# Kernel tuning notes

Hardware: AMD Instinct MI355X
Metric: run time of the kernel (lower is better)

The kernel has to match this reference:

```python
import jax, jax.numpy as jnp
import numpy as np
import math

S, B, H, NH = 2048, 2, 2048, 16
HN = H // NH  # 128, head dim


def _rope_cache(seq_len, hn):
    # inv_freqs over even indices, half_hn entries
    inv_freqs = 0.0001 ** (jnp.arange(0, hn, 2, dtype=jnp.float32) / hn)
    pos = jnp.arange(seq_len, dtype=jnp.float32)
    angles = pos[:, None] * inv_freqs  # [s, hn/2]
    return jnp.cos(angles), jnp.sin(angles)


def _apply_rope(x, cos, sin):
    # x: [s, b, np, hn]; cos/sin: [s, hn/2] broadcast over b, np
    half = x.shape[-1] // 2
    c = cos[:, None, None, :]
    s = sin[:, None, None, :]
    left, right = x[..., :half], x[..., half:]
    return jnp.concatenate((c * left - s * right, s * left + c * right), axis=-1)


def setup_inputs() -> dict:
    key = jax.random.key(0)
    k0, k1, k2 = jax.random.split(key, 3)
    hidden_states = jax.random.normal(k0, (S, B, H), dtype=jnp.float32)
    # causal additive mask, broadcast over batch and heads
    causal = jnp.tril(jnp.ones((S, S), dtype=bool))
    attention_mask = jnp.where(causal, 0.0, -1e9).astype(jnp.float32)[None, None]
    W_qkv = jax.random.normal(k1, (3 * H, H), dtype=jnp.float32) * 0.02
    b_qkv = jnp.zeros((3 * H,), dtype=jnp.float32)
    W_dense = jax.random.normal(k2, (H, H), dtype=jnp.float32) * 0.02
    b_dense = jnp.zeros((H,), dtype=jnp.float32)
    return {"hidden_states": hidden_states, "attention_mask": attention_mask,
            "W_qkv": W_qkv, "b_qkv": b_qkv, "W_dense": W_dense, "b_dense": b_dense}


def reference(hidden_states, attention_mask, W_qkv, b_qkv, W_dense, b_dense):
    s, b, h = hidden_states.shape
    # fused QKV projection: [s,b,3h] -> [s,b,np,3*hn] -> split per head
    mixed = hidden_states @ W_qkv.T + b_qkv
    mixed = mixed.reshape(s, b, NH, 3 * HN)
    q, k, v = jnp.split(mixed, 3, axis=-1)  # each [s,b,np,hn]
    cos, sin = _rope_cache(s, HN)
    q = _apply_rope(q, cos, sin)
    k = _apply_rope(k, cos, sin)
    norm_factor = math.sqrt(HN)  # coeff is None (scale_attn_by_inverse_layer_idx=False)
    scores = jnp.einsum('sbnh,tbnh->bnst', q, k) / norm_factor  # [b,np,sq,sk]
    scores = scores + attention_mask
    probs = jax.nn.softmax(scores, axis=-1)  # dropout p=0 in eval
    ctx = jnp.einsum('bnst,tbnh->sbnh', probs, v).reshape(s, b, h)
    return ctx @ W_dense.T + b_dense  # [s,b,h]
```

## Files before the change

kernel.cpp:

```cpp
#include <hip/hip_runtime.h>

#define SEQ   2048
#define BATCH 2
#define HID   2048
#define NHEAD 16
#define HDIM  128
#define MTOT  4096
#define KDIM  2048

typedef __attribute__((ext_vector_type(8))) short  bf16x8;
typedef __attribute__((ext_vector_type(4))) float  f32x4;
typedef __attribute__((ext_vector_type(4))) unsigned short u16x4;
typedef __attribute__((ext_vector_type(8))) unsigned short u16x8;

__device__ __forceinline__ unsigned short f2bf(float x) {
  unsigned u = __float_as_uint(x);
  u += 0x7fffu + ((u >> 16) & 1u);
  return (unsigned short)(u >> 16);
}

__device__ __forceinline__ float fexp2(float x) {
  float r;
  asm("v_exp_f32 %0, %1" : "=v"(r) : "v"(x));
  return r;
}

__device__ __forceinline__ void gl_lds16(const void* g, void* l) {
  __builtin_amdgcn_global_load_lds(
      (__attribute__((address_space(1))) void*)g,
      (__attribute__((address_space(3))) void*)l, 16, 0, 0);
}

__device__ __forceinline__ f32x4 mfma16(bf16x8 a, bf16x8 b, f32x4 c) {
  return __builtin_amdgcn_mfma_f32_16x16x32_bf16(a, b, c, 0, 0, 0);
}

__global__ __launch_bounds__(256, 8)
void prep(const float* __restrict__ hidden, const float* __restrict__ Wqkv,
          const float* __restrict__ Wd,
          unsigned short* __restrict__ hidb, unsigned short* __restrict__ wqkvb,
          unsigned short* __restrict__ wdb,
          float* __restrict__ cosT, float* __restrict__ sinT) {
  int bid = blockIdx.x;
  if (bid < 24576) {
    const float* src; unsigned short* dst; int lb;
    if (bid < 8192)       { src = hidden; dst = hidb;  lb = bid; }
    else if (bid < 20480) { src = Wqkv;   dst = wqkvb; lb = bid - 8192; }
    else                  { src = Wd;     dst = wdb;   lb = bid - 20480; }
    int i = lb * 256 + threadIdx.x;
    int base = i << 2;
    int r = base >> 11, k = base & 2047;
    f32x4 v = *(const f32x4*)(src + base);
    int kp = k ^ (((r >> 1) & 3) << 3);
    u16x4 o;
    o[0] = f2bf(v[0]); o[1] = f2bf(v[1]); o[2] = f2bf(v[2]); o[3] = f2bf(v[3]);
    *(u16x4*)(dst + (size_t)r * 2048 + kp) = o;
  } else {
    int idx = (bid - 24576) * 256 + threadIdx.x;
    int s = idx >> 6, i = idx & 63;
    float inv = powf(1e-4f, (float)i * (1.0f / 64.0f));
    float a = (float)s * inv;
    cosT[idx] = cosf(a);
    sinT[idx] = sinf(a);
  }
}

__global__ __launch_bounds__(512, 2)
void gemm_qkv(const unsigned short* __restrict__ A,
              const unsigned short* __restrict__ Bt,
              const float* __restrict__ bias,
              unsigned short* __restrict__ Qs,
              unsigned short* __restrict__ Ks,
              unsigned short* __restrict__ Vp,
              const float* __restrict__ cosT,
              const float* __restrict__ sinT)
{
  __shared__ alignas(16) char lds[98304];
  const int tid = threadIdx.x;
  const int wid = tid >> 6, lane = tid & 63, g = lane >> 4, c = lane & 15;
  const int wr = wid >> 2, wc = wid & 3;

  const int bid = blockIdx.x;
  const int swz = (bid & 7) * 64 + (bid >> 3);
  const int nblk = swz & 15, mblk = swz >> 4;
  const int m0 = mblk << 7;
  const int n0 = nblk * 384;
  const int nh = nblk;

  char* ldsb = (char*)lds;
  const int slotg = (g ^ ((c >> 1) & 3)) << 4;
  const char* ldsAr = ldsb + (wr * 64 + c) * 64 + slotg;
  const char* ldsBr = ldsb + 24576 + (wc * 16 + c) * 64 + slotg;

  const char* gA = (const char*)A  + (size_t)(m0 + (tid >> 2)) * 4096 + (tid & 3) * 16;
  const char* gB = (const char*)Bt + (size_t)(n0 + (tid >> 2)) * 4096 + (tid & 3) * 16;
  char* lA = ldsb + tid * 16;
  char* lB = ldsb + 24576 + tid * 16;

#define STG_A(T, BUF) gl_lds16(gA + (T) * 64, lA + (BUF) * 8192)
#define STG_B(T, BUF) do { const char* _g = gB + (T) * 64; char* _l = lB + (BUF) * 24576; \
    gl_lds16(_g, _l); gl_lds16(_g + 524288, _l + 8192); gl_lds16(_g + 1048576, _l + 16384); } while (0)

  f32x4 acc[4][6];
#pragma unroll
  for (int i = 0; i < 4; ++i)
#pragma unroll
    for (int j = 0; j < 6; ++j) {
      acc[i][j][0] = 0.f; acc[i][j][1] = 0.f; acc[i][j][2] = 0.f; acc[i][j][3] = 0.f;
    }

  bf16x8 a[4], b[6];
  const int NT = KDIM / 32;

#define TILE(T, BUF, BUFN) do {                                             \
    if ((T) + 2 < NT) { STG_A((T) + 2, BUFN); STG_B((T) + 2, BUFN); }       \
    _Pragma("unroll")                                                       \
    for (int mf = 0; mf < 4; ++mf)                                          \
      a[mf] = *(const bf16x8*)(ldsAr + (BUF) * 8192 + mf * 1024);           \
    _Pragma("unroll")                                                       \
    for (int nl = 0; nl < 6; ++nl)                                          \
      b[nl] = *(const bf16x8*)(ldsBr + (BUF) * 24576 + nl * 4096);          \
    __builtin_amdgcn_s_setprio(1);                                          \
    _Pragma("unroll")                                                       \
    for (int mf = 0; mf < 4; ++mf)                                          \
      _Pragma("unroll")                                                     \
      for (int nl = 0; nl < 6; ++nl)                                        \
        acc[mf][nl] = mfma16(a[mf], b[nl], acc[mf][nl]);                    \
    __builtin_amdgcn_s_setprio(0);                                          \
    if ((T) + 2 < NT) { asm volatile("s_waitcnt vmcnt(4)" ::: "memory"); }  \
    else              { asm volatile("s_waitcnt vmcnt(0)" ::: "memory"); }  \
    __builtin_amdgcn_s_barrier();                                           \
  } while (0)

  STG_A(0, 0); STG_B(0, 0);
  STG_A(1, 1); STG_B(1, 1);
  asm volatile("s_waitcnt vmcnt(4)" ::: "memory");
  __builtin_amdgcn_s_barrier();

  for (int t = 0; t < 63; t += 3) {
    TILE(t, 0, 2);
    TILE(t + 1, 1, 0);
    TILE(t + 2, 2, 1);
  }
  TILE(63, 0, 2);

  const float qsc = 0.08838834764831845f * 1.4426950408889634f;
  const int dl = wc * 16 + c;
#pragma unroll
  for (int ar = 0; ar < 4; ++ar) {
#pragma unroll
    for (int rr = 0; rr < 4; ++rr) {
      int m = m0 + wr * 64 + ar * 16 + g * 4 + rr;
      int s = m >> 1, bb = m & 1;
      size_t plane = (size_t)(bb * NHEAD + nh) * (SEQ * HDIM);
      int swb = (s & 7) << 3;
      float co = cosT[s * 64 + dl], si = sinT[s * 64 + dl];
      {
        float xl = acc[ar][0][rr] + bias[n0 + dl];
        float xr = acc[ar][1][rr] + bias[n0 + 64 + dl];
        Qs[plane + (size_t)s * HDIM + (dl ^ swb)]        = f2bf((co * xl - si * xr) * qsc);
        Qs[plane + (size_t)s * HDIM + ((dl + 64) ^ swb)] = f2bf((si * xl + co * xr) * qsc);
      }
      {
        float xl = acc[ar][2][rr] + bias[n0 + 128 + dl];
        float xr = acc[ar][3][rr] + bias[n0 + 192 + dl];
        Ks[plane + (size_t)s * HDIM + (dl ^ swb)]        = f2bf(co * xl - si * xr);
        Ks[plane + (size_t)s * HDIM + ((dl + 64) ^ swb)] = f2bf(si * xl + co * xr);
      }
      Vp[plane + (size_t)s * HDIM + dl]      = f2bf(acc[ar][4][rr] + bias[n0 + 256 + dl]);
      Vp[plane + (size_t)s * HDIM + dl + 64] = f2bf(acc[ar][5][rr] + bias[n0 + 320 + dl]);
    }
  }
#undef TILE
#undef STG_A
#undef STG_B
}

__global__ __launch_bounds__(512, 2)
void gemm_out(const unsigned short* __restrict__ A,
              const unsigned short* __restrict__ Bt,
              const float* __restrict__ bias,
              float* __restrict__ Cout)
{
  __shared__ alignas(16) char lds[73728];
  const int tid = threadIdx.x;
  const int wid = tid >> 6, lane = tid & 63, g = lane >> 4, c = lane & 15;
  const int wr = wid >> 2, wc = wid & 3;

  const int bid = blockIdx.x;
  const int swz = (bid & 7) * 32 + (bid >> 3);
  const int nblk = swz >> 5, mblk = swz & 31;
  const int m0 = mblk << 7, n0 = nblk << 8;

  char* ldsb = (char*)lds;
  const int slotg = (g ^ ((c >> 1) & 3)) << 4;
  const char* ldsAr = ldsb + (wr * 64 + c) * 64 + slotg;
  const char* ldsBr = ldsb + 24576 + (wc * 64 + c) * 64 + slotg;

  const char* gA = (const char*)A  + (size_t)(m0 + (tid >> 2)) * 4096 + (tid & 3) * 16;
  const char* gB = (const char*)Bt + (size_t)(n0 + (tid >> 2)) * 4096 + (tid & 3) * 16;
  char* lA = ldsb + tid * 16;
  char* lB = ldsb + 24576 + tid * 16;

#define STG_A(T, BUF) gl_lds16(gA + (T) * 64, lA + (BUF) * 8192)
#define STG_B(T, BUF) do { const char* _g = gB + (T) * 64; char* _l = lB + (BUF) * 16384; \
    gl_lds16(_g, _l); gl_lds16(_g + 524288, _l + 8192); } while (0)

  f32x4 acc[4][4];
#pragma unroll
  for (int i = 0; i < 4; ++i)
#pragma unroll
    for (int j = 0; j < 4; ++j) {
      acc[i][j][0] = 0.f; acc[i][j][1] = 0.f; acc[i][j][2] = 0.f; acc[i][j][3] = 0.f;
    }

  bf16x8 a[4], b[4];
  const int NT = KDIM / 32;

#define TILE(T, BUF, BUFN) do {                                             \
    if ((T) + 2 < NT) { STG_A((T) + 2, BUFN); STG_B((T) + 2, BUFN); }       \
    _Pragma("unroll")                                                       \
    for (int mf = 0; mf < 4; ++mf)                                          \
      a[mf] = *(const bf16x8*)(ldsAr + (BUF) * 8192 + mf * 1024);           \
    _Pragma("unroll")                                                       \
    for (int nl = 0; nl < 4; ++nl)                                          \
      b[nl] = *(const bf16x8*)(ldsBr + (BUF) * 16384 + nl * 1024);          \
    __builtin_amdgcn_s_setprio(1);                                          \
    _Pragma("unroll")                                                       \
    for (int mf = 0; mf < 4; ++mf)                                          \
      _Pragma("unroll")                                                     \
      for (int nl = 0; nl < 4; ++nl)                                        \
        acc[mf][nl] = mfma16(a[mf], b[nl], acc[mf][nl]);                    \
    __builtin_amdgcn_s_setprio(0);                                          \
    if ((T) + 2 < NT) { asm volatile("s_waitcnt vmcnt(3)" ::: "memory"); }  \
    else              { asm volatile("s_waitcnt vmcnt(0)" ::: "memory"); }  \
    __builtin_amdgcn_s_barrier();                                           \
  } while (0)

  STG_A(0, 0); STG_B(0, 0);
  STG_A(1, 1); STG_B(1, 1);
  asm volatile("s_waitcnt vmcnt(3)" ::: "memory");
  __builtin_amdgcn_s_barrier();

  for (int t = 0; t < 63; t += 3) {
    TILE(t, 0, 2);
    TILE(t + 1, 1, 0);
    TILE(t + 2, 2, 1);
  }
  TILE(63, 0, 2);

#pragma unroll
  for (int mf = 0; mf < 4; ++mf)
#pragma unroll
    for (int rr = 0; rr < 4; ++rr) {
      int m = m0 + wr * 64 + mf * 16 + g * 4 + rr;
#pragma unroll
      for (int nl = 0; nl < 4; ++nl) {
        int n = n0 + wc * 64 + nl * 16 + c;
        Cout[(size_t)m * HID + n] = acc[mf][nl][rr] + bias[n];
      }
    }
#undef TILE
#undef STG_A
#undef STG_B
}

__global__ __launch_bounds__(256, 4)
void transpose_v(const unsigned short* __restrict__ Vp, unsigned short* __restrict__ Vt) {
  __shared__ alignas(16) unsigned short T[64 * 136];
  const int plane = blockIdx.x >> 5;
  const int t0 = (blockIdx.x & 31) << 6;
  const size_t pbase = (size_t)plane * (SEQ * HDIM);
  const int tid = threadIdx.x;
  {
    int t = tid >> 2, d0 = (tid & 3) << 5;
    const unsigned short* src = Vp + pbase + (size_t)(t0 + t) * HDIM + d0;
#pragma unroll
    for (int j = 0; j < 4; ++j) {
      u16x8 v = *(const u16x8*)(src + j * 8);
      *(u16x8*)(&T[t * 136 + d0 + j * 8]) = v;
    }
  }
  __syncthreads();
  {
    int d = tid >> 1, half = tid & 1;
    unsigned short* dstp = Vt + pbase + (size_t)d * SEQ;
    int swb = (d & 7) << 3;
#pragma unroll
    for (int gg = 0; gg < 4; ++gg) {
      u16x8 v;
#pragma unroll
      for (int e = 0; e < 8; ++e)
        v[e] = T[(half * 32 + gg * 8 + e) * 136 + d];
      int tloc = half * 32 + gg * 8;
      *(u16x8*)(dstp + ((t0 + tloc) ^ swb)) = v;
    }
  }
}

__global__ __launch_bounds__(256, 2)
void attn(const unsigned short* __restrict__ Qs,
          const unsigned short* __restrict__ Ks,
          const unsigned short* __restrict__ Vt,
          unsigned short* __restrict__ ctx)
{
  __shared__ alignas(16) unsigned short Klds[2][64 * 128];
  __shared__ alignas(16) unsigned short Vlds[128 * 64];
  __shared__ alignas(16) unsigned short Plds[128 * 72];
  const int tid = threadIdx.x;
  const int w = tid >> 6, lane = tid & 63, g = lane >> 4, c = lane & 15;
  const int bid = blockIdx.x;
  const int head = bid & 31;
  const int qb = (bid < 256) ? (15 - (bid >> 5)) : ((bid >> 5) - 8);
  const int q0 = qb << 7;
  const size_t plane = (size_t)head * (SEQ * HDIM);
  const unsigned short* Qp = Qs + plane;
  const unsigned short* Kp = Ks + plane;
  const unsigned short* Vp = Vt + plane;

  bf16x8 qf[2][4];
#pragma unroll
  for (int q2 = 0; q2 < 2; ++q2) {
    int s = q0 + w * 32 + q2 * 16 + c;
    int swb = (s & 7) << 3;
#pragma unroll
    for (int kk = 0; kk < 4; ++kk) {
      int d0 = kk * 32 + g * 8;
      qf[q2][kk] = *(const bf16x8*)(Qp + (size_t)s * HDIM + (d0 ^ swb));
    }
  }

  f32x4 accO[2][8];
#pragma unroll
  for (int i = 0; i < 2; ++i)
#pragma unroll
    for (int j = 0; j < 8; ++j) {
      accO[i][j][0] = 0.f; accO[i][j][1] = 0.f; accO[i][j][2] = 0.f; accO[i][j][3] = 0.f;
    }
  float mrun[2] = { -1e30f, -1e30f };
  float lrun[2] = { 0.f, 0.f };

  const char* KgBase = (const char*)Kp + (tid >> 4) * 256 + (tid & 15) * 16;
  const char* VgBase = (const char*)Vp + (size_t)(tid >> 3) * 4096 + (tid & 7) * 16;
  char* VldsW = (char*)Vlds + w * 1024;

  const int ntiles = (q0 >> 6) + 2;
  const int qminw = q0 + w * 32;
  const int qmaxw = qminw + 31;

#pragma unroll
  for (int i = 0; i < 4; ++i)
    gl_lds16(KgBase, (char*)Klds[0] + w * 1024 + i * 4096), KgBase += 4096;
  KgBase -= 16384;

  for (int kt = 0; kt < ntiles; ++kt) {
    const int t0 = kt << 6;
    const bool havenext = (kt + 1 < ntiles);

#pragma unroll
    for (int i = 0; i < 4; ++i)
      gl_lds16(VgBase + t0 * 2 + (size_t)i * 131072, VldsW + i * 4096);
    if (havenext) {
      char* kdst = (char*)Klds[(kt + 1) & 1] + w * 1024;
#pragma unroll
      for (int i = 0; i < 4; ++i)
        gl_lds16(KgBase + (size_t)(t0 + 64) * 256 + i * 4096, kdst + i * 4096);
    }
    if (havenext) asm volatile("s_waitcnt vmcnt(8)" ::: "memory");
    else          asm volatile("s_waitcnt vmcnt(4)" ::: "memory");
    __builtin_amdgcn_s_barrier();

    if (t0 <= qmaxw) {
      const char* Kb = (const char*)Klds[kt & 1];
      f32x4 sacc[4][2];
#pragma unroll
      for (int i = 0; i < 4; ++i)
#pragma unroll
        for (int j = 0; j < 2; ++j) {
          sacc[i][j][0] = 0.f; sacc[i][j][1] = 0.f; sacc[i][j][2] = 0.f; sacc[i][j][3] = 0.f;
        }
      __builtin_amdgcn_s_setprio(1);
#pragma unroll
      for (int kk = 0; kk < 4; ++kk) {
        bf16x8 kf[4];
#pragma unroll
        for (int ta = 0; ta < 4; ++ta) {
          int t = ta * 16 + c;
          int d0 = kk * 32 + g * 8;
          kf[ta] = *(const bf16x8*)(Kb + t * 256 + ((d0 ^ ((t & 7) << 3)) << 1));
        }
#pragma unroll
        for (int ta = 0; ta < 4; ++ta)
#pragma unroll
          for (int q2 = 0; q2 < 2; ++q2)
            sacc[ta][q2] = mfma16(kf[ta], qf[q2][kk], sacc[ta][q2]);
      }
      __builtin_amdgcn_s_setprio(0);

      if (t0 + 63 > qminw) {
#pragma unroll
        for (int ta = 0; ta < 4; ++ta)
#pragma unroll
          for (int q2 = 0; q2 < 2; ++q2)
#pragma unroll
            for (int r = 0; r < 4; ++r) {
              int t = t0 + ta * 16 + g * 4 + r;
              int q = qminw + q2 * 16 + c;
              if (t > q) sacc[ta][q2][r] = -30000.f;
            }
      }

      float corr[2];
      bool resc = false;
#pragma unroll
      for (int q2 = 0; q2 < 2; ++q2) {
        float mx = -30000.f;
#pragma unroll
        for (int ta = 0; ta < 4; ++ta)
          mx = fmaxf(mx, fmaxf(fmaxf(sacc[ta][q2][0], sacc[ta][q2][1]),
                               fmaxf(sacc[ta][q2][2], sacc[ta][q2][3])));
        mx = fmaxf(mx, __shfl_xor(mx, 16));
        mx = fmaxf(mx, __shfl_xor(mx, 32));
        bool rs = mx > mrun[q2] + 8.0f;
        resc |= rs;
        float mnew = rs ? mx : mrun[q2];
        corr[q2] = fexp2(mrun[q2] - mnew);
        mrun[q2] = mnew;
        float ls = 0.f;
#pragma unroll
        for (int ta = 0; ta < 4; ++ta)
#pragma unroll
          for (int r = 0; r < 4; ++r) {
            float e = fexp2(sacc[ta][q2][r] - mnew);
            sacc[ta][q2][r] = e;
            ls += e;
          }
        ls += __shfl_xor(ls, 16);
        ls += __shfl_xor(ls, 32);
        lrun[q2] = lrun[q2] * corr[q2] + ls;
      }

      if (__any(resc)) {
#pragma unroll
        for (int q2 = 0; q2 < 2; ++q2)
#pragma unroll
          for (int r = 0; r < 4; ++r) {
            float cD = __shfl(corr[q2], (lane & 48) | (((lane >> 4) << 2) + r));
#pragma unroll
            for (int fn = 0; fn < 8; ++fn) accO[q2][fn][r] *= cD;
          }
      }

#pragma unroll
      for (int q2 = 0; q2 < 2; ++q2) {
        int prow = w * 32 + q2 * 16 + c;
#pragma unroll
        for (int ta = 0; ta < 4; ++ta) {
          u16x4 pk;
          pk[0] = f2bf(sacc[ta][q2][0]); pk[1] = f2bf(sacc[ta][q2][1]);
          pk[2] = f2bf(sacc[ta][q2][2]); pk[3] = f2bf(sacc[ta][q2][3]);
          *(u16x4*)(&Plds[prow * 72 + ta * 16 + g * 4]) = pk;
        }
      }
    }

    if (havenext) asm volatile("s_waitcnt vmcnt(4)" ::: "memory");
    else          asm volatile("s_waitcnt vmcnt(0)" ::: "memory");
    __builtin_amdgcn_s_barrier();

    if (t0 <= qmaxw) {
      __builtin_amdgcn_s_setprio(1);
#pragma unroll
      for (int kk = 0; kk < 2; ++kk) {
        bf16x8 pa[2];
#pragma unroll
        for (int q2 = 0; q2 < 2; ++q2)
          pa[q2] = *(const bf16x8*)((const char*)Plds + (w * 32 + q2 * 16 + c) * 144 + (kk * 32 + g * 8) * 2);
#pragma unroll
        for (int fn = 0; fn < 8; ++fn) {
          int d = fn * 16 + c;
          int tt = kk * 32 + g * 8;
          bf16x8 vb = *(const bf16x8*)((const char*)Vlds + d * 128 + ((tt ^ ((d & 7) << 3)) << 1));
#pragma unroll
          for (int q2 = 0; q2 < 2; ++q2)
            accO[q2][fn] = mfma16(pa[q2], vb, accO[q2][fn]);
        }
      }
      __builtin_amdgcn_s_setprio(0);
    }
    __builtin_amdgcn_s_barrier();
  }

  const int b = head >> 4, nh = head & 15;
  float linv[2] = { 1.0f / lrun[0], 1.0f / lrun[1] };
#pragma unroll
  for (int q2 = 0; q2 < 2; ++q2)
#pragma unroll
    for (int r = 0; r < 4; ++r) {
      float inv = __shfl(linv[q2], (lane & 48) | (((lane >> 4) << 2) + r));
      int q = q0 + w * 32 + q2 * 16 + g * 4 + r;
      int m = q * 2 + b;
      int swb = ((m >> 1) & 3) << 3;
#pragma unroll
      for (int fn = 0; fn < 8; ++fn) {
        int h = nh * 128 + fn * 16 + c;
        ctx[(size_t)m * HID + (h ^ swb)] = f2bf(accO[q2][fn][r] * inv);
      }
    }
}

extern "C" void kernel_launch(void* const* d_in, const int* in_sizes, int n_in,
                              void* d_out, int out_size, void* d_ws, size_t ws_size,
                              hipStream_t stream) {
  const float* hidden = (const float*)d_in[0];
  const float* Wqkv = (const float*)d_in[2];
  const float* bqkv = (const float*)d_in[3];
  const float* Wd   = (const float*)d_in[4];
  const float* bd   = (const float*)d_in[5];
  float* out = (float*)d_out;
  char* ws = (char*)d_ws;

  const size_t OFF_HID  = 0;
  const size_t OFF_WQKV = 16777216;
  const size_t OFF_WD   = 41943040;
  const size_t OFF_COS  = 50331648;
  const size_t OFF_SIN  = 50855936;
  const size_t OFF_Q    = 51380224;
  const size_t OFF_K    = 68157440;
  const size_t OFF_V    = 84934656;
  const size_t OFF_VT   = 101711872;
  if (ws_size < 118489088) return;

  unsigned short* hidb  = (unsigned short*)(ws + OFF_HID);
  unsigned short* wqkvb = (unsigned short*)(ws + OFF_WQKV);
  unsigned short* wdb   = (unsigned short*)(ws + OFF_WD);
  float* cosT = (float*)(ws + OFF_COS);
  float* sinT = (float*)(ws + OFF_SIN);
  unsigned short* Qsb = (unsigned short*)(ws + OFF_Q);
  unsigned short* Ksb = (unsigned short*)(ws + OFF_K);
  unsigned short* Vpb = (unsigned short*)(ws + OFF_V);
  unsigned short* Vtb = (unsigned short*)(ws + OFF_VT);
  unsigned short* ctxb = hidb;

  prep<<<25088, 256, 0, stream>>>(hidden, Wqkv, Wd, hidb, wqkvb, wdb, cosT, sinT);

  gemm_qkv<<<512, 512, 0, stream>>>(hidb, wqkvb, bqkv, Qsb, Ksb, Vpb, cosT, sinT);
  transpose_v<<<1024, 256, 0, stream>>>(Vpb, Vtb);
  attn<<<512, 256, 0, stream>>>(Qsb, Ksb, Vtb, ctxb);
  gemm_out<<<256, 512, 0, stream>>>(ctxb, wdb, bd, out);
}
```

Baseline: 249.4 us.

## Deepen GEMM pipelines to four LDS stages with register-double-buffered fragments

Both the QKV and output GEMMs move from a 3-stage to a 4-stage LDS ring, prefetching global tiles three steps ahead. They also ping-pong A/B fragment registers, loading the next tile's fragments from LDS before issuing the current tile's MFMAs, with a sched_barrier to keep that order. The aim is to hide global-to-LDS and LDS-read latency behind matrix work. The cost is more LDS per block: 128KB for QKV and 96KB for out-proj. That may cut resident blocks per CU, especially for gemm_out. It also adds register pressure from doubled fragment arrays.

```diff
diff --git a/kernel.cpp b/kernel.cpp
--- a/kernel.cpp
+++ b/kernel.cpp
@@ -75,7 +75,7 @@
               const float* __restrict__ cosT,
               const float* __restrict__ sinT)
 {
-  __shared__ alignas(16) char lds[98304];
+  __shared__ alignas(16) char lds[131072];
   const int tid = threadIdx.x;
   const int wid = tid >> 6, lane = tid & 63, g = lane >> 4, c = lane & 15;
   const int wr = wid >> 2, wc = wid & 3;
@@ -90,12 +90,12 @@
   char* ldsb = (char*)lds;
   const int slotg = (g ^ ((c >> 1) & 3)) << 4;
   const char* ldsAr = ldsb + (wr * 64 + c) * 64 + slotg;
-  const char* ldsBr = ldsb + 24576 + (wc * 16 + c) * 64 + slotg;
+  const char* ldsBr = ldsb + 32768 + (wc * 16 + c) * 64 + slotg;
 
   const char* gA = (const char*)A  + (size_t)(m0 + (tid >> 2)) * 4096 + (tid & 3) * 16;
   const char* gB = (const char*)Bt + (size_t)(n0 + (tid >> 2)) * 4096 + (tid & 3) * 16;
   char* lA = ldsb + tid * 16;
-  char* lB = ldsb + 24576 + tid * 16;
+  char* lB = ldsb + 32768 + tid * 16;
 
 #define STG_A(T, BUF) gl_lds16(gA + (T) * 64, lA + (BUF) * 8192)
 #define STG_B(T, BUF) do { const char* _g = gB + (T) * 64; char* _l = lB + (BUF) * 24576; \
@@ -109,40 +109,47 @@
       acc[i][j][0] = 0.f; acc[i][j][1] = 0.f; acc[i][j][2] = 0.f; acc[i][j][3] = 0.f;
     }
 
-  bf16x8 a[4], b[6];
+  bf16x8 a0[4], b0[6], a1[4], b1[6];
   const int NT = KDIM / 32;
 
-#define TILE(T, BUF, BUFN) do {                                             \
-    if ((T) + 2 < NT) { STG_A((T) + 2, BUFN); STG_B((T) + 2, BUFN); }       \
+#define FRAGQ(BUF, AR, BR) do {                                             \
     _Pragma("unroll")                                                       \
     for (int mf = 0; mf < 4; ++mf)                                          \
-      a[mf] = *(const bf16x8*)(ldsAr + (BUF) * 8192 + mf * 1024);           \
+      AR[mf] = *(const bf16x8*)(ldsAr + (BUF) * 8192 + mf * 1024);          \
     _Pragma("unroll")                                                       \
     for (int nl = 0; nl < 6; ++nl)                                          \
-      b[nl] = *(const bf16x8*)(ldsBr + (BUF) * 24576 + nl * 4096);          \
+      BR[nl] = *(const bf16x8*)(ldsBr + (BUF) * 24576 + nl * 4096);         \
+  } while (0)
+
+#define TILEQ(T, BUFS, BUFN, AC, BC, AN, BN) do {                           \
+    if ((T) + 3 < NT) { STG_A((T) + 3, BUFS); STG_B((T) + 3, BUFS); }       \
+    if ((T) + 1 < NT) { FRAGQ(BUFN, AN, BN); }                              \
+    __builtin_amdgcn_sched_barrier(0);                                      \
     __builtin_amdgcn_s_setprio(1);                                          \
     _Pragma("unroll")                                                       \
     for (int mf = 0; mf < 4; ++mf)                                          \
       _Pragma("unroll")                                                     \
       for (int nl = 0; nl < 6; ++nl)                                        \
-        acc[mf][nl] = mfma16(a[mf], b[nl], acc[mf][nl]);                    \
+        acc[mf][nl] = mfma16(AC[mf], BC[nl], acc[mf][nl]);                  \
     __builtin_amdgcn_s_setprio(0);                                          \
-    if ((T) + 2 < NT) { asm volatile("s_waitcnt vmcnt(4)" ::: "memory"); }  \
-    else              { asm volatile("s_waitcnt vmcnt(0)" ::: "memory"); }  \
+    if ((T) + 3 < NT) { asm volatile("s_waitcnt vmcnt(4) lgkmcnt(0)" ::: "memory"); } \
+    else              { asm volatile("s_waitcnt vmcnt(0) lgkmcnt(0)" ::: "memory"); } \
     __builtin_amdgcn_s_barrier();                                           \
   } while (0)
 
   STG_A(0, 0); STG_B(0, 0);
   STG_A(1, 1); STG_B(1, 1);
+  STG_A(2, 2); STG_B(2, 2);
   asm volatile("s_waitcnt vmcnt(4)" ::: "memory");
   __builtin_amdgcn_s_barrier();
-
-  for (int t = 0; t < 63; t += 3) {
-    TILE(t, 0, 2);
-    TILE(t + 1, 1, 0);
-    TILE(t + 2, 2, 1);
-  }
-  TILE(63, 0, 2);
+  FRAGQ(0, a0, b0);
+
+  for (int t = 0; t < NT; t += 4) {
+    TILEQ(t + 0, 3, 1, a0, b0, a1, b1);
+    TILEQ(t + 1, 0, 2, a1, b1, a0, b0);
+    TILEQ(t + 2, 1, 3, a0, b0, a1, b1);
+    TILEQ(t + 3, 2, 0, a1, b1, a0, b0);
+  }
 
   const float qsc = 0.08838834764831845f * 1.4426950408889634f;
   const int dl = wc * 16 + c;
@@ -171,7 +178,8 @@
       Vp[plane + (size_t)s * HDIM + dl + 64] = f2bf(acc[ar][5][rr] + bias[n0 + 320 + dl]);
     }
   }
-#undef TILE
+#undef TILEQ
+#undef FRAGQ
 #undef STG_A
 #undef STG_B
 }
@@ -182,7 +190,7 @@
               const float* __restrict__ bias,
               float* __restrict__ Cout)
 {
-  __shared__ alignas(16) char lds[73728];
+  __shared__ alignas(16) char lds[98304];
   const int tid = threadIdx.x;
   const int wid = tid >> 6, lane = tid & 63, g = lane >> 4, c = lane & 15;
   const int wr = wid >> 2, wc = wid & 3;
@@ -195,12 +203,12 @@
   char* ldsb = (char*)lds;
   const int slotg = (g ^ ((c >> 1) & 3)) << 4;
   const char* ldsAr = ldsb + (wr * 64 + c) * 64 + slotg;
-  const char* ldsBr = ldsb + 24576 + (wc * 64 + c) * 64 + slotg;
+  const char* ldsBr = ldsb + 32768 + (wc * 64 + c) * 64 + slotg;
 
   const char* gA = (const char*)A  + (size_t)(m0 + (tid >> 2)) * 4096 + (tid & 3) * 16;
   const char* gB = (const char*)Bt + (size_t)(n0 + (tid >> 2)) * 4096 + (tid & 3) * 16;
   char* lA = ldsb + tid * 16;
-  char* lB = ldsb + 24576 + tid * 16;
+  char* lB = ldsb + 32768 + tid * 16;
 
 #define STG_A(T, BUF) gl_lds16(gA + (T) * 64, lA + (BUF) * 8192)
 #define STG_B(T, BUF) do { const char* _g = gB + (T) * 64; char* _l = lB + (BUF) * 16384; \
@@ -214,40 +222,47 @@
       acc[i][j][0] = 0.f; acc[i][j][1] = 0.f; acc[i][j][2] = 0.f; acc[i][j][3] = 0.f;
     }
 
-  bf16x8 a[4], b[4];
+  bf16x8 a0[4], b0[4], a1[4], b1[4];
   const int NT = KDIM / 32;
 
-#define TILE(T, BUF, BUFN) do {                                             \
-    if ((T) + 2 < NT) { STG_A((T) + 2, BUFN); STG_B((T) + 2, BUFN); }       \
+#define FRAGO(BUF, AR, BR) do {                                             \
     _Pragma("unroll")                                                       \
     for (int mf = 0; mf < 4; ++mf)                                          \
-      a[mf] = *(const bf16x8*)(ldsAr + (BUF) * 8192 + mf * 1024);           \
+      AR[mf] = *(const bf16x8*)(ldsAr + (BUF) * 8192 + mf * 1024);          \
     _Pragma("unroll")                                                       \
     for (int nl = 0; nl < 4; ++nl)                                          \
-      b[nl] = *(const bf16x8*)(ldsBr + (BUF) * 16384 + nl * 1024);          \
+      BR[nl] = *(const bf16x8*)(ldsBr + (BUF) * 16384 + nl * 1024);         \
+  } while (0)
+
+#define TILEO(T, BUFS, BUFN, AC, BC, AN, BN) do {                           \
+    if ((T) + 3 < NT) { STG_A((T) + 3, BUFS); STG_B((T) + 3, BUFS); }       \
+    if ((T) + 1 < NT) { FRAGO(BUFN, AN, BN); }                              \
+    __builtin_amdgcn_sched_barrier(0);                                      \
     __builtin_amdgcn_s_setprio(1);                                          \
     _Pragma("unroll")                                                       \
     for (int mf = 0; mf < 4; ++mf)                                          \
       _Pragma("unroll")                                                     \
       for (int nl = 0; nl < 4; ++nl)                                        \
-        acc[mf][nl] = mfma16(a[mf], b[nl], acc[mf][nl]);                    \
+        acc[mf][nl] = mfma16(AC[mf], BC[nl], acc[mf][nl]);                  \
     __builtin_amdgcn_s_setprio(0);                                          \
-    if ((T) + 2 < NT) { asm volatile("s_waitcnt vmcnt(3)" ::: "memory"); }  \
-    else              { asm volatile("s_waitcnt vmcnt(0)" ::: "memory"); }  \
+    if ((T) + 3 < NT) { asm volatile("s_waitcnt vmcnt(3) lgkmcnt(0)" ::: "memory"); } \
+    else              { asm volatile("s_waitcnt vmcnt(0) lgkmcnt(0)" ::: "memory"); } \
     __builtin_amdgcn_s_barrier();                                           \
   } while (0)
 
   STG_A(0, 0); STG_B(0, 0);
   STG_A(1, 1); STG_B(1, 1);
+  STG_A(2, 2); STG_B(2, 2);
   asm volatile("s_waitcnt vmcnt(3)" ::: "memory");
   __builtin_amdgcn_s_barrier();
-
-  for (int t = 0; t < 63; t += 3) {
-    TILE(t, 0, 2);
-    TILE(t + 1, 1, 0);
-    TILE(t + 2, 2, 1);
-  }
-  TILE(63, 0, 2);
+  FRAGO(0, a0, b0);
+
+  for (int t = 0; t < NT; t += 4) {
+    TILEO(t + 0, 3, 1, a0, b0, a1, b1);
+    TILEO(t + 1, 0, 2, a1, b1, a0, b0);
+    TILEO(t + 2, 1, 3, a0, b0, a1, b1);
+    TILEO(t + 3, 2, 0, a1, b1, a0, b0);
+  }
 
 #pragma unroll
   for (int mf = 0; mf < 4; ++mf)
@@ -260,7 +275,8 @@
         Cout[(size_t)m * HID + n] = acc[mf][nl][rr] + bias[n];
       }
     }
-#undef TILE
+#undef TILEO
+#undef FRAGO
 #undef STG_A
 #undef STG_B
 }
```

New measurement: 249.9 us. No clear change (+0.2%).

## Load GEMM A operand directly into registers, bypassing LDS

Applied to the files above, without the earlier changes.

In both the QKV and output GEMMs, the A operand now goes straight from global memory into registers with a three-deep register ring, instead of being staged through LDS. The hidden-state and context buffers are therefore no longer XOR-swizzled, and the attention epilogue and prep kernel change to match. LDS use shrinks and the B fragment reads move to just after the barrier so they overlap better. The cost is more VGPRs and uncoalesced per-lane global loads of A, which may hurt occupancy or memory efficiency.

```diff
diff --git a/kernel.cpp b/kernel.cpp
--- a/kernel.cpp
+++ b/kernel.cpp
@@ -43,15 +43,15 @@
           float* __restrict__ cosT, float* __restrict__ sinT) {
   int bid = blockIdx.x;
   if (bid < 24576) {
-    const float* src; unsigned short* dst; int lb;
-    if (bid < 8192)       { src = hidden; dst = hidb;  lb = bid; }
-    else if (bid < 20480) { src = Wqkv;   dst = wqkvb; lb = bid - 8192; }
-    else                  { src = Wd;     dst = wdb;   lb = bid - 20480; }
+    const float* src; unsigned short* dst; int lb; bool swz;
+    if (bid < 8192)       { src = hidden; dst = hidb;  lb = bid;         swz = false; }
+    else if (bid < 20480) { src = Wqkv;   dst = wqkvb; lb = bid - 8192;  swz = true; }
+    else                  { src = Wd;     dst = wdb;   lb = bid - 20480; swz = true; }
     int i = lb * 256 + threadIdx.x;
     int base = i << 2;
     int r = base >> 11, k = base & 2047;
     f32x4 v = *(const f32x4*)(src + base);
-    int kp = k ^ (((r >> 1) & 3) << 3);
+    int kp = swz ? (k ^ (((r >> 1) & 3) << 3)) : k;
     u16x4 o;
     o[0] = f2bf(v[0]); o[1] = f2bf(v[1]); o[2] = f2bf(v[2]); o[3] = f2bf(v[3]);
     *(u16x4*)(dst + (size_t)r * 2048 + kp) = o;
@@ -75,7 +75,7 @@
               const float* __restrict__ cosT,
               const float* __restrict__ sinT)
 {
-  __shared__ alignas(16) char lds[98304];
+  __shared__ alignas(16) char lds[73728];
   const int tid = threadIdx.x;
   const int wid = tid >> 6, lane = tid & 63, g = lane >> 4, c = lane & 15;
   const int wr = wid >> 2, wc = wid & 3;
@@ -89,17 +89,21 @@
 
   char* ldsb = (char*)lds;
   const int slotg = (g ^ ((c >> 1) & 3)) << 4;
-  const char* ldsAr = ldsb + (wr * 64 + c) * 64 + slotg;
-  const char* ldsBr = ldsb + 24576 + (wc * 16 + c) * 64 + slotg;
-
-  const char* gA = (const char*)A  + (size_t)(m0 + (tid >> 2)) * 4096 + (tid & 3) * 16;
+  const char* ldsBr = ldsb + (wc * 16 + c) * 64 + slotg;
+
+  const char* gA2 = (const char*)A + (size_t)(m0 + wr * 64 + c) * 4096 + g * 16;
   const char* gB = (const char*)Bt + (size_t)(n0 + (tid >> 2)) * 4096 + (tid & 3) * 16;
-  char* lA = ldsb + tid * 16;
-  char* lB = ldsb + 24576 + tid * 16;
-
-#define STG_A(T, BUF) gl_lds16(gA + (T) * 64, lA + (BUF) * 8192)
+  char* lB = ldsb + tid * 16;
+
 #define STG_B(T, BUF) do { const char* _g = gB + (T) * 64; char* _l = lB + (BUF) * 24576; \
     gl_lds16(_g, _l); gl_lds16(_g + 524288, _l + 8192); gl_lds16(_g + 1048576, _l + 16384); } while (0)
+#define A_LOAD(T, AR) do { const char* _g = gA2 + (T) * 64;                  \
+    _Pragma("unroll")                                                        \
+    for (int mf = 0; mf < 4; ++mf)                                           \
+      AR[mf] = *(const bf16x8*)(_g + mf * 65536); } while (0)
+#define FRAG_B(BUF) do { _Pragma("unroll")                                   \
+    for (int nl = 0; nl < 6; ++nl)                                           \
+      b[nl] = *(const bf16x8*)(ldsBr + (BUF) * 24576 + nl * 4096); } while (0)
 
   f32x4 acc[4][6];
 #pragma unroll
@@ -109,40 +113,38 @@
       acc[i][j][0] = 0.f; acc[i][j][1] = 0.f; acc[i][j][2] = 0.f; acc[i][j][3] = 0.f;
     }
 
-  bf16x8 a[4], b[6];
+  bf16x8 a0[4], a1[4], a2[4], b[6];
   const int NT = KDIM / 32;
 
-#define TILE(T, BUF, BUFN) do {                                             \
-    if ((T) + 2 < NT) { STG_A((T) + 2, BUFN); STG_B((T) + 2, BUFN); }       \
-    _Pragma("unroll")                                                       \
-    for (int mf = 0; mf < 4; ++mf)                                          \
-      a[mf] = *(const bf16x8*)(ldsAr + (BUF) * 8192 + mf * 1024);           \
-    _Pragma("unroll")                                                       \
-    for (int nl = 0; nl < 6; ++nl)                                          \
-      b[nl] = *(const bf16x8*)(ldsBr + (BUF) * 24576 + nl * 4096);          \
-    __builtin_amdgcn_s_setprio(1);                                          \
-    _Pragma("unroll")                                                       \
-    for (int mf = 0; mf < 4; ++mf)                                          \
-      _Pragma("unroll")                                                     \
-      for (int nl = 0; nl < 6; ++nl)                                        \
-        acc[mf][nl] = mfma16(a[mf], b[nl], acc[mf][nl]);                    \
-    __builtin_amdgcn_s_setprio(0);                                          \
-    if ((T) + 2 < NT) { asm volatile("s_waitcnt vmcnt(4)" ::: "memory"); }  \
-    else              { asm volatile("s_waitcnt vmcnt(0)" ::: "memory"); }  \
-    __builtin_amdgcn_s_barrier();                                           \
+#define TILEQ(T, BUFS, BUFR, AC, AN) do {                                    \
+    if ((T) + 2 < NT) { STG_B((T) + 2, BUFS); A_LOAD((T) + 2, AN); }         \
+    asm volatile("s_waitcnt lgkmcnt(0)" ::: "memory");                       \
+    __builtin_amdgcn_sched_barrier(0);                                       \
+    __builtin_amdgcn_s_setprio(1);                                           \
+    _Pragma("unroll")                                                        \
+    for (int mf = 0; mf < 4; ++mf)                                           \
+      _Pragma("unroll")                                                      \
+      for (int nl = 0; nl < 6; ++nl)                                         \
+        acc[mf][nl] = mfma16(AC[mf], b[nl], acc[mf][nl]);                    \
+    __builtin_amdgcn_s_setprio(0);                                           \
+    if ((T) + 2 < NT) { asm volatile("s_waitcnt vmcnt(7)" ::: "memory"); }   \
+    else              { asm volatile("s_waitcnt vmcnt(0)" ::: "memory"); }   \
+    __builtin_amdgcn_s_barrier();                                            \
+    if ((T) + 1 < NT) { FRAG_B(BUFR); }                                      \
   } while (0)
 
-  STG_A(0, 0); STG_B(0, 0);
-  STG_A(1, 1); STG_B(1, 1);
-  asm volatile("s_waitcnt vmcnt(4)" ::: "memory");
+  STG_B(0, 0); A_LOAD(0, a0);
+  STG_B(1, 1); A_LOAD(1, a1);
+  asm volatile("s_waitcnt vmcnt(7)" ::: "memory");
   __builtin_amdgcn_s_barrier();
+  FRAG_B(0);
 
   for (int t = 0; t < 63; t += 3) {
-    TILE(t, 0, 2);
-    TILE(t + 1, 1, 0);
-    TILE(t + 2, 2, 1);
-  }
-  TILE(63, 0, 2);
+    TILEQ(t,     2, 1, a0, a2);
+    TILEQ(t + 1, 0, 2, a1, a0);
+    TILEQ(t + 2, 1, 0, a2, a1);
+  }
+  TILEQ(63, 2, 1, a0, a2);
 
   const float qsc = 0.08838834764831845f * 1.4426950408889634f;
   const int dl = wc * 16 + c;
@@ -171,8 +173,9 @@
       Vp[plane + (size_t)s * HDIM + dl + 64] = f2bf(acc[ar][5][rr] + bias[n0 + 320 + dl]);
     }
   }
-#undef TILE
-#undef STG_A
+#undef TILEQ
+#undef FRAG_B
+#undef A_LOAD
 #undef STG_B
 }
 
@@ -182,7 +185,7 @@
               const float* __restrict__ bias,
               float* __restrict__ Cout)
 {
-  __shared__ alignas(16) char lds[73728];
+  __shared__ alignas(16) char lds[49152];
   const int tid = threadIdx.x;
   const int wid = tid >> 6, lane = tid & 63, g = lane >> 4, c = lane & 15;
   const int wr = wid >> 2, wc = wid & 3;
@@ -194,17 +197,21 @@
 
   char* ldsb = (char*)lds;
   const int slotg = (g ^ ((c >> 1) & 3)) << 4;
-  const char* ldsAr = ldsb + (wr * 64 + c) * 64 + slotg;
-  const char* ldsBr = ldsb + 24576 + (wc * 64 + c) * 64 + slotg;
-
-  const char* gA = (const char*)A  + (size_t)(m0 + (tid >> 2)) * 4096 + (tid & 3) * 16;
+  const char* ldsBr = ldsb + (wc * 64 + c) * 64 + slotg;
+
+  const char* gA2 = (const char*)A + (size_t)(m0 + wr * 64 + c) * 4096 + g * 16;
   const char* gB = (const char*)Bt + (size_t)(n0 + (tid >> 2)) * 4096 + (tid & 3) * 16;
-  char* lA = ldsb + tid * 16;
-  char* lB = ldsb + 24576 + tid * 16;
-
-#define STG_A(T, BUF) gl_lds16(gA + (T) * 64, lA + (BUF) * 8192)
+  char* lB = ldsb + tid * 16;
+
 #define STG_B(T, BUF) do { const char* _g = gB + (T) * 64; char* _l = lB + (BUF) * 16384; \
     gl_lds16(_g, _l); gl_lds16(_g + 524288, _l + 8192); } while (0)
+#define A_LOAD(T, AR) do { const char* _g = gA2 + (T) * 64;                  \
+    _Pragma("unroll")                                                        \
+    for (int mf = 0; mf < 4; ++mf)                                           \
+      AR[mf] = *(const bf16x8*)(_g + mf * 65536); } while (0)
+#define FRAG_B(BUF) do { _Pragma("unroll")                                   \
+    for (int nl = 0; nl < 4; ++nl)                                           \
+      b[nl] = *(const bf16x8*)(ldsBr + (BUF) * 16384 + nl * 1024); } while (0)
 
   f32x4 acc[4][4];
 #pragma unroll
@@ -214,40 +221,38 @@
       acc[i][j][0] = 0.f; acc[i][j][1] = 0.f; acc[i][j][2] = 0.f; acc[i][j][3] = 0.f;
     }
 
-  bf16x8 a[4], b[4];
+  bf16x8 a0[4], a1[4], a2[4], b[4];
   const int NT = KDIM / 32;
 
-#define TILE(T, BUF, BUFN) do {                                             \
-    if ((T) + 2 < NT) { STG_A((T) + 2, BUFN); STG_B((T) + 2, BUFN); }       \
-    _Pragma("unroll")                                                       \
-    for (int mf = 0; mf < 4; ++mf)                                          \
-      a[mf] = *(const bf16x8*)(ldsAr + (BUF) * 8192 + mf * 1024);           \
-    _Pragma("unroll")                                                       \
-    for (int nl = 0; nl < 4; ++nl)                                          \
-      b[nl] = *(const bf16x8*)(ldsBr + (BUF) * 16384 + nl * 1024);          \
-    __builtin_amdgcn_s_setprio(1);                                          \
-    _Pragma("unroll")                                                       \
-    for (int mf = 0; mf < 4; ++mf)                                          \
-      _Pragma("unroll")                                                     \
-      for (int nl = 0; nl < 4; ++nl)                                        \
-        acc[mf][nl] = mfma16(a[mf], b[nl], acc[mf][nl]);                    \
-    __builtin_amdgcn_s_setprio(0);                                          \
-    if ((T) + 2 < NT) { asm volatile("s_waitcnt vmcnt(3)" ::: "memory"); }  \
-    else              { asm volatile("s_waitcnt vmcnt(0)" ::: "memory"); }  \
-    __builtin_amdgcn_s_barrier();                                           \
+#define TILEO(T, BUFS, BUFR, AC, AN) do {                                    \
+    if ((T) + 2 < NT) { STG_B((T) + 2, BUFS); A_LOAD((T) + 2, AN); }         \
+    asm volatile("s_waitcnt lgkmcnt(0)" ::: "memory");                       \
+    __builtin_amdgcn_sched_barrier(0);                                       \
+    __builtin_amdgcn_s_setprio(1);                                           \
+    _Pragma("unroll")                                                        \
+    for (int mf = 0; mf < 4; ++mf)                                           \
+      _Pragma("unroll")                                                      \
+      for (int nl = 0; nl < 4; ++nl)                                         \
+        acc[mf][nl] = mfma16(AC[mf], b[nl], acc[mf][nl]);                    \
+    __builtin_amdgcn_s_setprio(0);                                           \
+    if ((T) + 2 < NT) { asm volatile("s_waitcnt vmcnt(6)" ::: "memory"); }   \
+    else              { asm volatile("s_waitcnt vmcnt(0)" ::: "memory"); }   \
+    __builtin_amdgcn_s_barrier();                                            \
+    if ((T) + 1 < NT) { FRAG_B(BUFR); }                                      \
   } while (0)
 
-  STG_A(0, 0); STG_B(0, 0);
-  STG_A(1, 1); STG_B(1, 1);
-  asm volatile("s_waitcnt vmcnt(3)" ::: "memory");
+  STG_B(0, 0); A_LOAD(0, a0);
+  STG_B(1, 1); A_LOAD(1, a1);
+  asm volatile("s_waitcnt vmcnt(6)" ::: "memory");
   __builtin_amdgcn_s_barrier();
+  FRAG_B(0);
 
   for (int t = 0; t < 63; t += 3) {
-    TILE(t, 0, 2);
-    TILE(t + 1, 1, 0);
-    TILE(t + 2, 2, 1);
-  }
-  TILE(63, 0, 2);
+    TILEO(t,     2, 1, a0, a2);
+    TILEO(t + 1, 0, 2, a1, a0);
+    TILEO(t + 2, 1, 0, a2, a1);
+  }
+  TILEO(63, 2, 1, a0, a2);
 
 #pragma unroll
   for (int mf = 0; mf < 4; ++mf)
@@ -260,8 +265,9 @@
         Cout[(size_t)m * HID + n] = acc[mf][nl][rr] + bias[n];
       }
     }
-#undef TILE
-#undef STG_A
+#undef TILEO
+#undef FRAG_B
+#undef A_LOAD
 #undef STG_B
 }
 
@@ -500,11 +506,10 @@
       float inv = __shfl(linv[q2], (lane & 48) | (((lane >> 4) << 2) + r));
       int q = q0 + w * 32 + q2 * 16 + g * 4 + r;
       int m = q * 2 + b;
-      int swb = ((m >> 1) & 3) << 3;
 #pragma unroll
       for (int fn = 0; fn < 8; ++fn) {
         int h = nh * 128 + fn * 16 + c;
-        ctx[(size_t)m * HID + (h ^ swb)] = f2bf(accO[q2][fn][r] * inv);
+        ctx[(size_t)m * HID + h] = f2bf(accO[q2][fn][r] * inv);
       }
     }
 }
```

New measurement: 359.3 us. 1.44x slower.

## Pair complementary causal query blocks per 512-thread attention workgroup sharing K/V tiles

Applied to the files above, without the earlier changes.

Each attention workgroup now has 8 waves covering two query blocks of the same head: a late block (15-j) and its early complement (j). The two blocks share one stream of K/V LDS tiles, so K/V global traffic per head is cut and the causal work per workgroup is balanced. Global-to-LDS loads are spread over 512 threads with adjusted vmcnt waits, and the launch uses half as many blocks. The cost is that the early-block waves sit idle through the later tiles while still joining the barriers, and the larger LDS footprint may limit occupancy.

```diff
diff --git a/kernel.cpp b/kernel.cpp
--- a/kernel.cpp
+++ b/kernel.cpp
@@ -298,7 +298,7 @@
   }
 }
 
-__global__ __launch_bounds__(256, 2)
+__global__ __launch_bounds__(512, 2)
 void attn(const unsigned short* __restrict__ Qs,
           const unsigned short* __restrict__ Ks,
           const unsigned short* __restrict__ Vt,
@@ -306,22 +306,21 @@
 {
   __shared__ alignas(16) unsigned short Klds[2][64 * 128];
   __shared__ alignas(16) unsigned short Vlds[128 * 64];
-  __shared__ alignas(16) unsigned short Plds[128 * 72];
+  __shared__ alignas(16) unsigned short Plds[256 * 72];
   const int tid = threadIdx.x;
   const int w = tid >> 6, lane = tid & 63, g = lane >> 4, c = lane & 15;
   const int bid = blockIdx.x;
   const int head = bid & 31;
-  const int qb = (bid < 256) ? (15 - (bid >> 5)) : ((bid >> 5) - 8);
-  const int q0 = qb << 7;
+  const int j = bid >> 5;
+  const int qbh = 15 - j;
+  const int q0w = (w < 4) ? ((qbh << 7) + w * 32) : ((j << 7) + (w - 4) * 32);
   const size_t plane = (size_t)head * (SEQ * HDIM);
   const unsigned short* Qp = Qs + plane;
-  const unsigned short* Kp = Ks + plane;
-  const unsigned short* Vp = Vt + plane;
 
   bf16x8 qf[2][4];
 #pragma unroll
   for (int q2 = 0; q2 < 2; ++q2) {
-    int s = q0 + w * 32 + q2 * 16 + c;
+    int s = q0w + q2 * 16 + c;
     int swb = (s & 7) << 3;
 #pragma unroll
     for (int kk = 0; kk < 4; ++kk) {
@@ -334,40 +333,35 @@
 #pragma unroll
   for (int i = 0; i < 2; ++i)
 #pragma unroll
-    for (int j = 0; j < 8; ++j) {
-      accO[i][j][0] = 0.f; accO[i][j][1] = 0.f; accO[i][j][2] = 0.f; accO[i][j][3] = 0.f;
+    for (int jj = 0; jj < 8; ++jj) {
+      accO[i][jj][0] = 0.f; accO[i][jj][1] = 0.f; accO[i][jj][2] = 0.f; accO[i][jj][3] = 0.f;
     }
   float mrun[2] = { -1e30f, -1e30f };
   float lrun[2] = { 0.f, 0.f };
 
-  const char* KgBase = (const char*)Kp + (tid >> 4) * 256 + (tid & 15) * 16;
-  const char* VgBase = (const char*)Vp + (size_t)(tid >> 3) * 4096 + (tid & 7) * 16;
-  char* VldsW = (char*)Vlds + w * 1024;
-
-  const int ntiles = (q0 >> 6) + 2;
-  const int qminw = q0 + w * 32;
-  const int qmaxw = qminw + 31;
-
-#pragma unroll
-  for (int i = 0; i < 4; ++i)
-    gl_lds16(KgBase, (char*)Klds[0] + w * 1024 + i * 4096), KgBase += 4096;
-  KgBase -= 16384;
+  const char* Kg = (const char*)(Ks + plane) + (tid >> 4) * 256 + (tid & 15) * 16;
+  const char* Vg = (const char*)(Vt + plane) + (size_t)(tid >> 3) * 4096 + (tid & 7) * 16;
+
+  const int ntiles = (qbh << 1) + 2;
+  const int qminw = q0w;
+  const int qmaxw = q0w + 31;
+
+  gl_lds16(Kg,        (char*)Klds[0] + tid * 16);
+  gl_lds16(Kg + 8192, (char*)Klds[0] + tid * 16 + 8192);
 
   for (int kt = 0; kt < ntiles; ++kt) {
     const int t0 = kt << 6;
     const bool havenext = (kt + 1 < ntiles);
 
-#pragma unroll
-    for (int i = 0; i < 4; ++i)
-      gl_lds16(VgBase + t0 * 2 + (size_t)i * 131072, VldsW + i * 4096);
+    gl_lds16(Vg + t0 * 2,          (char*)Vlds + tid * 16);
+    gl_lds16(Vg + t0 * 2 + 262144, (char*)Vlds + tid * 16 + 8192);
     if (havenext) {
-      char* kdst = (char*)Klds[(kt + 1) & 1] + w * 1024;
-#pragma unroll
-      for (int i = 0; i < 4; ++i)
-        gl_lds16(KgBase + (size_t)(t0 + 64) * 256 + i * 4096, kdst + i * 4096);
-    }
-    if (havenext) asm volatile("s_waitcnt vmcnt(8)" ::: "memory");
-    else          asm volatile("s_waitcnt vmcnt(4)" ::: "memory");
+      char* kd = (char*)Klds[(kt + 1) & 1] + tid * 16;
+      gl_lds16(Kg + (size_t)(t0 + 64) * 256,        kd);
+      gl_lds16(Kg + (size_t)(t0 + 64) * 256 + 8192, kd + 8192);
+    }
+    if (havenext) asm volatile("s_waitcnt vmcnt(4)" ::: "memory");
+    else          asm volatile("s_waitcnt vmcnt(2)" ::: "memory");
     __builtin_amdgcn_s_barrier();
 
     if (t0 <= qmaxw) {
@@ -376,8 +370,8 @@
 #pragma unroll
       for (int i = 0; i < 4; ++i)
 #pragma unroll
-        for (int j = 0; j < 2; ++j) {
-          sacc[i][j][0] = 0.f; sacc[i][j][1] = 0.f; sacc[i][j][2] = 0.f; sacc[i][j][3] = 0.f;
+        for (int jj = 0; jj < 2; ++jj) {
+          sacc[i][jj][0] = 0.f; sacc[i][jj][1] = 0.f; sacc[i][jj][2] = 0.f; sacc[i][jj][3] = 0.f;
         }
       __builtin_amdgcn_s_setprio(1);
 #pragma unroll
@@ -464,7 +458,7 @@
       }
     }
 
-    if (havenext) asm volatile("s_waitcnt vmcnt(4)" ::: "memory");
+    if (havenext) asm volatile("s_waitcnt vmcnt(2)" ::: "memory");
     else          asm volatile("s_waitcnt vmcnt(0)" ::: "memory");
     __builtin_amdgcn_s_barrier();
 
@@ -498,7 +492,7 @@
 #pragma unroll
     for (int r = 0; r < 4; ++r) {
       float inv = __shfl(linv[q2], (lane & 48) | (((lane >> 4) << 2) + r));
-      int q = q0 + w * 32 + q2 * 16 + g * 4 + r;
+      int q = q0w + q2 * 16 + g * 4 + r;
       int m = q * 2 + b;
       int swb = ((m >> 1) & 3) << 3;
 #pragma unroll
@@ -546,6 +540,6 @@
 
   gemm_qkv<<<512, 512, 0, stream>>>(hidb, wqkvb, bqkv, Qsb, Ksb, Vpb, cosT, sinT);
   transpose_v<<<1024, 256, 0, stream>>>(Vpb, Vtb);
-  attn<<<512, 256, 0, stream>>>(Qsb, Ksb, Vtb, ctxb);
+  attn<<<256, 512, 0, stream>>>(Qsb, Ksb, Vtb, ctxb);
   gemm_out<<<256, 512, 0, stream>>>(ctxb, wdb, bd, out);
 }
```

Measured after the change: 250.8 us. No clear change (+0.5%).
